# Performance work log

Hardware: AMD Instinct MI355X
Metric: run time of the kernel (lower is better)

## Reference

```python
import jax, jax.numpy as jnp
import numpy as np

N_USER = 10000
U_DIM = 256
IMG_DIM = 2048
W_DIM = 512
H_DIM = 1024
VOC = 32000
CAP_LEN = 64
SOS = VOC - 2  # <SOS> token id (n_voc_size - 2, as in the torch code)


def setup_inputs() -> dict:
    key = jax.random.key(0)
    ks = jax.random.split(key, 10)
    s = lambda k, shape: jax.random.normal(k, shape, jnp.float32) * 0.02
    return {
        "img_feat": jax.random.normal(ks[0], (1, IMG_DIM), jnp.float32),
        "uid": jax.random.randint(ks[1], (1,), 0, N_USER),
        "wei_user": s(ks[2], (N_USER, U_DIM)),
        "WI_w": s(ks[3], (W_DIM, IMG_DIM + U_DIM)),
        "WI_b": jnp.zeros((W_DIM,), jnp.float32),
        "WP_w": s(ks[4], (VOC, H_DIM)),
        "WP_b": jnp.zeros((VOC,), jnp.float32),
        "W_ih": s(ks[5], (4 * H_DIM, W_DIM)),
        "W_hh": s(ks[6], (4 * H_DIM, H_DIM)),
        "b_ih": jnp.zeros((4 * H_DIM,), jnp.float32),
        "b_hh": jnp.zeros((4 * H_DIM,), jnp.float32),
        "word_emb": s(ks[7], (VOC, W_DIM)),
    }


def _lstm_step(x, h, c, W_ih, W_hh, b_ih, b_hh):
    # torch nn.LSTM gate order: input, forget, cell(g), output
    gates = x @ W_ih.T + b_ih + h @ W_hh.T + b_hh  # [1, 4H]
    i, f, g, o = jnp.split(gates, 4, axis=-1)
    c = jax.nn.sigmoid(f) * c + jax.nn.sigmoid(i) * jnp.tanh(g)
    h = jax.nn.sigmoid(o) * jnp.tanh(c)
    return h, c


def reference(img_feat, uid, wei_user, WI_w, WI_b, WP_w, WP_b,
              W_ih, W_hh, b_ih, b_hh, word_emb):
    # user embedding + image feature -> conditioning input for step 0
    user_emb = wei_user[uid]                                  # [1, U_DIM]
    x0 = jnp.concatenate([img_feat, user_emb], axis=1) @ WI_w.T + WI_b  # [1, W_DIM]

    h = jnp.zeros((1, H_DIM), x0.dtype)
    c = jnp.zeros((1, H_DIM), x0.dtype)
    # prime the LSTM with the image/user conditioning vector
    h, c = _lstm_step(x0, h, c, W_ih, W_hh, b_ih, b_hh)

    def step(carry, _):
        h, c, wid = carry
        x = word_emb[wid]                                     # [1, W_DIM] embedding gather
        h, c = _lstm_step(x, h, c, W_ih, W_hh, b_ih, b_hh)
        logits = h @ WP_w.T + WP_b                            # [1, VOC]
        wid = jnp.argmax(logits, axis=-1).astype(jnp.int32)   # greedy token
        return (h, c, wid), (h, wid[0])

    wid0 = jnp.full((1,), SOS, jnp.int32)
    _, (hiddens, captions) = jax.lax.scan(step, (h, c, wid0), None, length=CAP_LEN)
    # hiddens: [CAP_LEN, 1, H_DIM] (matches torch cat of per-step LSTM outputs)
    return hiddens, captions
```

## Files before the change

### kernel.cpp

```cpp
#include <hip/hip_runtime.h>
#include <hip/hip_bf16.h>
#include <math.h>

#define H_DIM 1024
#define W_DIM 512
#define VOC 32000
#define CAP_LEN 64
#define U_DIM 256
#define IMG_DIM 2048
#define XIN_DIM (IMG_DIM + U_DIM)
#define SOS 31998
#define NBLK_LOGITS 512


__device__ __forceinline__ float wave_reduce_sum(float v) {
    #pragma unroll
    for (int off = 32; off > 0; off >>= 1)
        v += __shfl_xor(v, off, 64);
    return v;
}

__device__ __forceinline__ unsigned long long umax64(unsigned long long a, unsigned long long b) {
    return a > b ? a : b;
}

__device__ __forceinline__ unsigned short f2bf_rne(float f) {
    unsigned u = __float_as_uint(f);
    unsigned rounding = 0x7FFFu + ((u >> 16) & 1u);
    return (unsigned short)((u + rounding) >> 16);
}
__device__ __forceinline__ float bflo(unsigned u) { return __uint_as_float(u << 16); }
__device__ __forceinline__ float bfhi(unsigned u) { return __uint_as_float(u & 0xFFFF0000u); }

__global__ void k_init(const float* __restrict__ img, const int* __restrict__ uid,
                       const float* __restrict__ wei_user, float* __restrict__ wsf) {
    int i = blockIdx.x * blockDim.x + threadIdx.x;
    if (i < 4096) wsf[i] = 0.f;
    if (i < XIN_DIM) {
        float v = (i < IMG_DIM) ? img[i]
                                : wei_user[(size_t)uid[0] * U_DIM + (i - IMG_DIM)];
        wsf[4096 + i] = v;
    }
}

__global__ void k_cvt_wp(const float* __restrict__ src, ushort* __restrict__ dst) {
    int i = blockIdx.x * blockDim.x + threadIdx.x;
    const float4 a = reinterpret_cast<const float4*>(src)[2 * i];
    const float4 b = reinterpret_cast<const float4*>(src)[2 * i + 1];
    union { ushort s[8]; uint4 v; } u;
    u.s[0] = f2bf_rne(a.x); u.s[1] = f2bf_rne(a.y);
    u.s[2] = f2bf_rne(a.z); u.s[3] = f2bf_rne(a.w);
    u.s[4] = f2bf_rne(b.x); u.s[5] = f2bf_rne(b.y);
    u.s[6] = f2bf_rne(b.z); u.s[7] = f2bf_rne(b.w);
    reinterpret_cast<uint4*>(dst)[i] = u.v;
}

__global__ void k_x0(const float* __restrict__ WI_w, const float* __restrict__ WI_b,
                     const float* __restrict__ xin, float* __restrict__ x0) {
    int wave = threadIdx.x >> 6;
    int lane = threadIdx.x & 63;
    int row  = blockIdx.x * 4 + wave;
    const float* wr = WI_w + (size_t)row * XIN_DIM;
    float acc = 0.f;
    #pragma unroll
    for (int k = 0; k < 9; ++k) {
        int col = 4 * lane + 256 * k;
        float4 w4 = *reinterpret_cast<const float4*>(wr  + col);
        float4 v4 = *reinterpret_cast<const float4*>(xin + col);
        acc += w4.x * v4.x + w4.y * v4.y + w4.z * v4.z + w4.w * v4.w;
    }
    acc = wave_reduce_sum(acc);
    if (lane == 0) x0[row] = acc + WI_b[row];
}

__global__ void k_lstm(int t,
                       const float* __restrict__ W_ih, const float* __restrict__ W_hh,
                       const float* __restrict__ b_ih, const float* __restrict__ b_hh,
                       const float* __restrict__ word_emb, const float* __restrict__ x0,
                       const unsigned long long* __restrict__ partial,
                       float* __restrict__ out_cap,
                       const float* __restrict__ h_in, const float* __restrict__ c_in,
                       float* __restrict__ h_out, float* __restrict__ c_out,
                       float* __restrict__ out_hid) {
    __shared__ unsigned long long red[256];
    int tid  = threadIdx.x;
    int wave = tid >> 6;
    int lane = tid & 63;
    int j = blockIdx.x * 4 + wave;

    const float* x;
    if (t < 0) {
        x = x0;
    } else if (t == 0) {
        x = word_emb + (size_t)SOS * W_DIM;
    } else {
        unsigned long long b = umax64(partial[tid], partial[tid + 256]);
        red[tid] = b;
        __syncthreads();
        #pragma unroll
        for (int s = 128; s >= 1; s >>= 1) {
            if (tid < s) red[tid] = umax64(red[tid], red[tid + s]);
            __syncthreads();
        }
        int wid = (int)(0xFFFFFFFFu - (unsigned)(red[0] & 0xFFFFFFFFull));
        if (blockIdx.x == 0 && tid == 0) out_cap[t - 1] = (float)wid;
        x = word_emb + (size_t)wid * W_DIM;
    }

    float g[4];
    #pragma unroll
    for (int gi = 0; gi < 4; ++gi) {
        int row = gi * H_DIM + j;
        const float* wi = W_ih + (size_t)row * W_DIM;
        const float* wh = W_hh + (size_t)row * H_DIM;
        float acc = 0.f;
        #pragma unroll
        for (int k = 0; k < 2; ++k) {
            int col = 4 * lane + 256 * k;
            float4 w4 = *reinterpret_cast<const float4*>(wi + col);
            float4 v4 = *reinterpret_cast<const float4*>(x  + col);
            acc += w4.x * v4.x + w4.y * v4.y + w4.z * v4.z + w4.w * v4.w;
        }
        #pragma unroll
        for (int k = 0; k < 4; ++k) {
            int col = 4 * lane + 256 * k;
            float4 w4 = *reinterpret_cast<const float4*>(wh   + col);
            float4 v4 = *reinterpret_cast<const float4*>(h_in + col);
            acc += w4.x * v4.x + w4.y * v4.y + w4.z * v4.z + w4.w * v4.w;
        }
        acc = wave_reduce_sum(acc);
        g[gi] = acc + b_ih[row] + b_hh[row];
    }
    if (lane == 0) {
        float ig = 1.f / (1.f + expf(-g[0]));
        float fg = 1.f / (1.f + expf(-g[1]));
        float gg = tanhf(g[2]);
        float og = 1.f / (1.f + expf(-g[3]));
        float cn = fg * c_in[j] + ig * gg;
        float hn = og * tanhf(cn);
        c_out[j] = cn;
        h_out[j] = hn;
        if (out_hid) out_hid[j] = hn;
    }
}

__global__ void k_logits_bf16(const ushort* __restrict__ WP16,
                              const float* __restrict__ WP_b,
                              const float* __restrict__ h,
                              unsigned long long* __restrict__ partial) {
    int wave = threadIdx.x >> 6;
    int lane = threadIdx.x & 63;
    int wv = blockIdx.x * 4 + wave;
    float4 h0a = *reinterpret_cast<const float4*>(h + 8 * lane);
    float4 h0b = *reinterpret_cast<const float4*>(h + 8 * lane + 4);
    float4 h1a = *reinterpret_cast<const float4*>(h + 8 * lane + 512);
    float4 h1b = *reinterpret_cast<const float4*>(h + 8 * lane + 516);
    unsigned long long best = 0ull;
    for (int row = wv; row < VOC; row += NBLK_LOGITS * 4) {
        const uint4* wr = reinterpret_cast<const uint4*>(WP16 + (size_t)row * H_DIM);
        uint4 w0 = wr[lane];
        uint4 w1 = wr[lane + 64];
        float acc;
        acc  = bflo(w0.x) * h0a.x + bfhi(w0.x) * h0a.y;
        acc += bflo(w0.y) * h0a.z + bfhi(w0.y) * h0a.w;
        acc += bflo(w0.z) * h0b.x + bfhi(w0.z) * h0b.y;
        acc += bflo(w0.w) * h0b.z + bfhi(w0.w) * h0b.w;
        acc += bflo(w1.x) * h1a.x + bfhi(w1.x) * h1a.y;
        acc += bflo(w1.y) * h1a.z + bfhi(w1.y) * h1a.w;
        acc += bflo(w1.z) * h1b.x + bfhi(w1.z) * h1b.y;
        acc += bflo(w1.w) * h1b.z + bfhi(w1.w) * h1b.w;
        acc = wave_reduce_sum(acc);
        float logit = acc + WP_b[row];
        unsigned int ub = __float_as_uint(logit);
        ub = (ub & 0x80000000u) ? ~ub : (ub | 0x80000000u);
        unsigned long long p = ((unsigned long long)ub << 32)
                             | (unsigned long long)(0xFFFFFFFFu - (unsigned)row);
        best = umax64(best, p);
    }
    __shared__ unsigned long long sm[4];
    if (lane == 0) sm[wave] = best;
    __syncthreads();
    if (threadIdx.x == 0) {
        unsigned long long m = umax64(umax64(sm[0], sm[1]), umax64(sm[2], sm[3]));
        partial[blockIdx.x] = m;
    }
}

__global__ void k_logits_f32(const float* __restrict__ WP_w, const float* __restrict__ WP_b,
                             const float* __restrict__ h,
                             unsigned long long* __restrict__ partial) {
    int wave = threadIdx.x >> 6;
    int lane = threadIdx.x & 63;
    int wv = blockIdx.x * 4 + wave;
    unsigned long long best = 0ull;
    for (int row = wv; row < VOC; row += NBLK_LOGITS * 4) {
        const float* wr = WP_w + (size_t)row * H_DIM;
        float acc = 0.f;
        #pragma unroll
        for (int k = 0; k < 4; ++k) {
            int col = 4 * lane + 256 * k;
            float4 w4 = *reinterpret_cast<const float4*>(wr + col);
            float4 v4 = *reinterpret_cast<const float4*>(h  + col);
            acc += w4.x * v4.x + w4.y * v4.y + w4.z * v4.z + w4.w * v4.w;
        }
        acc = wave_reduce_sum(acc);
        float logit = acc + WP_b[row];
        unsigned int ub = __float_as_uint(logit);
        ub = (ub & 0x80000000u) ? ~ub : (ub | 0x80000000u);
        unsigned long long p = ((unsigned long long)ub << 32)
                             | (unsigned long long)(0xFFFFFFFFu - (unsigned)row);
        best = umax64(best, p);
    }
    __shared__ unsigned long long sm[4];
    if (lane == 0) sm[wave] = best;
    __syncthreads();
    if (threadIdx.x == 0) {
        unsigned long long m = umax64(umax64(sm[0], sm[1]), umax64(sm[2], sm[3]));
        partial[blockIdx.x] = m;
    }
}

__global__ void k_argmax_final(const unsigned long long* __restrict__ partial,
                               float* __restrict__ out_cap) {
    __shared__ unsigned long long sm[256];
    int tid = threadIdx.x;
    sm[tid] = umax64(partial[tid], partial[tid + 256]);
    __syncthreads();
    for (int s = 128; s > 0; s >>= 1) {
        if (tid < s) sm[tid] = umax64(sm[tid], sm[tid + s]);
        __syncthreads();
    }
    if (tid == 0) {
        int row = (int)(0xFFFFFFFFu - (unsigned)(sm[0] & 0xFFFFFFFFull));
        out_cap[CAP_LEN - 1] = (float)row;
    }
}

extern "C" void kernel_launch(void* const* d_in, const int* in_sizes, int n_in,
                              void* d_out, int out_size, void* d_ws, size_t ws_size,
                              hipStream_t stream) {
    const float* img_feat = (const float*)d_in[0];
    const int*   uid      = (const int*)  d_in[1];
    const float* wei_user = (const float*)d_in[2];
    const float* WI_w     = (const float*)d_in[3];
    const float* WI_b     = (const float*)d_in[4];
    const float* WP_w     = (const float*)d_in[5];
    const float* WP_b     = (const float*)d_in[6];
    const float* W_ih     = (const float*)d_in[7];
    const float* W_hh     = (const float*)d_in[8];
    const float* b_ih     = (const float*)d_in[9];
    const float* b_hh     = (const float*)d_in[10];
    const float* word_emb = (const float*)d_in[11];

    float* out = (float*)d_out;
    float* wsf = (float*)d_ws;
    float* h0 = wsf;
    float* h1 = wsf + 1024;
    float* c0 = wsf + 2048;
    float* c1 = wsf + 3072;
    float* xin = wsf + 4096;
    float* x0  = wsf + 6400;
    unsigned long long* partial = (unsigned long long*)((char*)d_ws + 27904);
    ushort* WP16 = (ushort*)((char*)d_ws + (1 << 20));
    const size_t wp16_need = (1u << 20) + (size_t)VOC * H_DIM * sizeof(ushort);
    const bool use_bf16 = ws_size >= wp16_need;

    if (use_bf16)
        k_cvt_wp<<<16000, 256, 0, stream>>>(WP_w, WP16);
    k_init<<<16, 256, 0, stream>>>(img_feat, uid, wei_user, wsf);
    k_x0<<<128, 256, 0, stream>>>(WI_w, WI_b, xin, x0);

    float* out_cap = out + CAP_LEN * H_DIM;

    k_lstm<<<256, 256, 0, stream>>>(-1, W_ih, W_hh, b_ih, b_hh, word_emb, x0,
                                    partial, out_cap, h0, c0, h1, c1, nullptr);

    for (int t = 0; t < CAP_LEN; ++t) {
        const float* hi = (t & 1) ? h0 : h1;
        const float* ci = (t & 1) ? c0 : c1;
        float* ho = (t & 1) ? h1 : h0;
        float* co = (t & 1) ? c1 : c0;
        k_lstm<<<256, 256, 0, stream>>>(t, W_ih, W_hh, b_ih, b_hh, word_emb, x0,
                                        partial, out_cap, hi, ci, ho, co,
                                        out + (size_t)t * H_DIM);
        if (use_bf16)
            k_logits_bf16<<<NBLK_LOGITS, 256, 0, stream>>>(WP16, WP_b, ho, partial);
        else
            k_logits_f32<<<NBLK_LOGITS, 256, 0, stream>>>(WP_w, WP_b, ho, partial);
    }
    k_argmax_final<<<1, 256, 0, stream>>>(partial, out_cap);
}
```

Before: 1.327 ms.

## Screen vocab logits with int8 weights and bound, rescore candidates in bf16

Adds an int8 per-row quantized copy of the projection weights with a per-row error norm. Each step first screens all rows with int8 dot products, using a Cauchy-Schwarz error bound to keep only rows that could be the argmax, then rescores those candidates exactly in bf16. The goal is to cut the per-step vocab weight traffic roughly in half. The LSTM kernel also moves to one block per hidden unit with one wave per gate. In exchange it adds a one-time quantize pass and more launches per step. The fallback path has bugs: it reduces only 256 of 512 partials and calls a stray memset.

New measurement: 1.435 ms. 1.08x slower.

```diff
diff --git a/kernel.cpp b/kernel.cpp
--- a/kernel.cpp
+++ b/kernel.cpp
@@ -11,12 +11,29 @@
 #define XIN_DIM (IMG_DIM + U_DIM)
 #define SOS 31998
 #define NBLK_LOGITS 512
-
+#define NSCR 1024
+#define NRESC 125
+
+#define WSF_OFF    16384
+#define PART_OFF   44288
+#define PLOW_OFF   46080
+#define ABUF_OFF   65536
+#define WP16_OFF   (1u << 20)
+#define WQ8_OFF    (96u << 20)
+#define META_OFF   (132u << 20)
+#define WS_NEED    ((size_t)(133u << 20))
 
 __device__ __forceinline__ float wave_reduce_sum(float v) {
     #pragma unroll
     for (int off = 32; off > 0; off >>= 1)
         v += __shfl_xor(v, off, 64);
+    return v;
+}
+
+__device__ __forceinline__ float wave_reduce_fmax(float v) {
+    #pragma unroll
+    for (int off = 32; off > 0; off >>= 1)
+        v = fmaxf(v, __shfl_xor(v, off, 64));
     return v;
 }
 
@@ -32,15 +49,34 @@
 __device__ __forceinline__ float bflo(unsigned u) { return __uint_as_float(u << 16); }
 __device__ __forceinline__ float bfhi(unsigned u) { return __uint_as_float(u & 0xFFFF0000u); }
 
-__global__ void k_init(const float* __restrict__ img, const int* __restrict__ uid,
-                       const float* __restrict__ wei_user, float* __restrict__ wsf) {
-    int i = blockIdx.x * blockDim.x + threadIdx.x;
-    if (i < 4096) wsf[i] = 0.f;
-    if (i < XIN_DIM) {
-        float v = (i < IMG_DIM) ? img[i]
-                                : wei_user[(size_t)uid[0] * U_DIM + (i - IMG_DIM)];
-        wsf[4096 + i] = v;
-    }
+__device__ __forceinline__ unsigned long long pack_key(float logit, int row) {
+    unsigned int ub = __float_as_uint(logit);
+    ub = (ub & 0x80000000u) ? ~ub : (ub | 0x80000000u);
+    return ((unsigned long long)ub << 32)
+         | (unsigned long long)(0xFFFFFFFFu - (unsigned)row);
+}
+
+__device__ __forceinline__ float lstm_row_dot(const float* __restrict__ wi,
+                                              const float* __restrict__ wh,
+                                              const float* __restrict__ x,
+                                              const float* __restrict__ h_in,
+                                              int lane) {
+    float acc = 0.f;
+    #pragma unroll
+    for (int k = 0; k < 2; ++k) {
+        int col = 4 * lane + 256 * k;
+        float4 w4 = *reinterpret_cast<const float4*>(wi + col);
+        float4 v4 = *reinterpret_cast<const float4*>(x  + col);
+        acc += w4.x * v4.x + w4.y * v4.y + w4.z * v4.z + w4.w * v4.w;
+    }
+    #pragma unroll
+    for (int k = 0; k < 4; ++k) {
+        int col = 4 * lane + 256 * k;
+        float4 w4 = *reinterpret_cast<const float4*>(wh   + col);
+        float4 v4 = *reinterpret_cast<const float4*>(h_in + col);
+        acc += w4.x * v4.x + w4.y * v4.y + w4.z * v4.z + w4.w * v4.w;
+    }
+    return wave_reduce_sum(acc);
 }
 
 __global__ void k_cvt_wp(const float* __restrict__ src, ushort* __restrict__ dst) {
@@ -55,6 +91,60 @@
     reinterpret_cast<uint4*>(dst)[i] = u.v;
 }
 
+__global__ void k_quant(const ushort* __restrict__ WP16, char* __restrict__ WQ8,
+                        float2* __restrict__ meta) {
+    int wave = threadIdx.x >> 6;
+    int lane = threadIdx.x & 63;
+    int gwv = blockIdx.x * 4 + wave;
+    for (int row = gwv; row < VOC; row += 4000) {
+        const uint4* wr = reinterpret_cast<const uint4*>(WP16 + (size_t)row * H_DIM);
+        uint4 w0 = wr[lane];
+        uint4 w1 = wr[lane + 64];
+        float v[16];
+        v[0] = bflo(w0.x); v[1] = bfhi(w0.x); v[2]  = bflo(w0.y); v[3]  = bfhi(w0.y);
+        v[4] = bflo(w0.z); v[5] = bfhi(w0.z); v[6]  = bflo(w0.w); v[7]  = bfhi(w0.w);
+        v[8] = bflo(w1.x); v[9] = bfhi(w1.x); v[10] = bflo(w1.y); v[11] = bfhi(w1.y);
+        v[12] = bflo(w1.z); v[13] = bfhi(w1.z); v[14] = bflo(w1.w); v[15] = bfhi(w1.w);
+        float mx = 0.f;
+        #pragma unroll
+        for (int i = 0; i < 16; ++i) mx = fmaxf(mx, fabsf(v[i]));
+        mx = wave_reduce_fmax(mx);
+        float s = mx / 127.f;
+        float inv = (s > 0.f) ? 1.f / s : 0.f;
+        int q[16];
+        float r2 = 0.f;
+        #pragma unroll
+        for (int i = 0; i < 16; ++i) {
+            float qq = rintf(v[i] * inv);
+            qq = fminf(127.f, fmaxf(-127.f, qq));
+            q[i] = (int)qq;
+            float res = v[i] - s * qq;
+            r2 += res * res;
+        }
+        r2 = wave_reduce_sum(r2);
+        float n = sqrtf(r2) * 1.0005f;
+        #define PK(a,b,c,d) (unsigned)((q[a]&0xff)|((q[b]&0xff)<<8)|((q[c]&0xff)<<16)|((q[d]&0xff)<<24))
+        uint2 lo = make_uint2(PK(0,1,2,3), PK(4,5,6,7));
+        uint2 hi = make_uint2(PK(8,9,10,11), PK(12,13,14,15));
+        #undef PK
+        char* rowp = WQ8 + (size_t)row * H_DIM;
+        *reinterpret_cast<uint2*>(rowp + 8 * lane)       = lo;
+        *reinterpret_cast<uint2*>(rowp + 512 + 8 * lane) = hi;
+        if (lane == 0) meta[row] = make_float2(s, n);
+    }
+}
+
+__global__ void k_init(const float* __restrict__ img, const int* __restrict__ uid,
+                       const float* __restrict__ wei_user, float* __restrict__ wsf) {
+    int i = blockIdx.x * blockDim.x + threadIdx.x;
+    if (i < 4096) wsf[i] = 0.f;
+    if (i < XIN_DIM) {
+        float v = (i < IMG_DIM) ? img[i]
+                                : wei_user[(size_t)uid[0] * U_DIM + (i - IMG_DIM)];
+        wsf[4096 + i] = v;
+    }
+}
+
 __global__ void k_x0(const float* __restrict__ WI_w, const float* __restrict__ WI_b,
                      const float* __restrict__ xin, float* __restrict__ x0) {
     int wave = threadIdx.x >> 6;
@@ -73,20 +163,21 @@
     if (lane == 0) x0[row] = acc + WI_b[row];
 }
 
-__global__ void k_lstm(int t,
-                       const float* __restrict__ W_ih, const float* __restrict__ W_hh,
-                       const float* __restrict__ b_ih, const float* __restrict__ b_hh,
-                       const float* __restrict__ word_emb, const float* __restrict__ x0,
-                       const unsigned long long* __restrict__ partial,
-                       float* __restrict__ out_cap,
-                       const float* __restrict__ h_in, const float* __restrict__ c_in,
-                       float* __restrict__ h_out, float* __restrict__ c_out,
-                       float* __restrict__ out_hid) {
+__global__ void k_lstm_b(int t,
+                         const float* __restrict__ W_ih, const float* __restrict__ W_hh,
+                         const float* __restrict__ b_ih, const float* __restrict__ b_hh,
+                         const float* __restrict__ word_emb, const float* __restrict__ x0,
+                         const unsigned long long* __restrict__ partial, int npart,
+                         float* __restrict__ out_cap,
+                         const float* __restrict__ h_in, const float* __restrict__ c_in,
+                         float* __restrict__ h_out, float* __restrict__ c_out,
+                         float* __restrict__ out_hid) {
     __shared__ unsigned long long red[256];
+    __shared__ float gsm[4];
     int tid  = threadIdx.x;
     int wave = tid >> 6;
     int lane = tid & 63;
-    int j = blockIdx.x * 4 + wave;
+    int j = blockIdx.x;
 
     const float* x;
     if (t < 0) {
@@ -94,8 +185,7 @@
     } else if (t == 0) {
         x = word_emb + (size_t)SOS * W_DIM;
     } else {
-        unsigned long long b = umax64(partial[tid], partial[tid + 256]);
-        red[tid] = b;
+        red[tid] = (tid < npart) ? partial[tid] : 0ull;
         __syncthreads();
         #pragma unroll
         for (int s = 128; s >= 1; s >>= 1) {
@@ -107,40 +197,153 @@
         x = word_emb + (size_t)wid * W_DIM;
     }
 
-    float g[4];
-    #pragma unroll
-    for (int gi = 0; gi < 4; ++gi) {
-        int row = gi * H_DIM + j;
-        const float* wi = W_ih + (size_t)row * W_DIM;
-        const float* wh = W_hh + (size_t)row * H_DIM;
-        float acc = 0.f;
-        #pragma unroll
-        for (int k = 0; k < 2; ++k) {
-            int col = 4 * lane + 256 * k;
-            float4 w4 = *reinterpret_cast<const float4*>(wi + col);
-            float4 v4 = *reinterpret_cast<const float4*>(x  + col);
-            acc += w4.x * v4.x + w4.y * v4.y + w4.z * v4.z + w4.w * v4.w;
-        }
-        #pragma unroll
-        for (int k = 0; k < 4; ++k) {
-            int col = 4 * lane + 256 * k;
-            float4 w4 = *reinterpret_cast<const float4*>(wh   + col);
-            float4 v4 = *reinterpret_cast<const float4*>(h_in + col);
-            acc += w4.x * v4.x + w4.y * v4.y + w4.z * v4.z + w4.w * v4.w;
-        }
-        acc = wave_reduce_sum(acc);
-        g[gi] = acc + b_ih[row] + b_hh[row];
-    }
-    if (lane == 0) {
-        float ig = 1.f / (1.f + expf(-g[0]));
-        float fg = 1.f / (1.f + expf(-g[1]));
-        float gg = tanhf(g[2]);
-        float og = 1.f / (1.f + expf(-g[3]));
+    int row = wave * H_DIM + j;
+    float acc = lstm_row_dot(W_ih + (size_t)row * W_DIM,
+                             W_hh + (size_t)row * H_DIM, x, h_in, lane);
+    float g = acc + b_ih[row] + b_hh[row];
+    if (lane == 0) gsm[wave] = g;
+    __syncthreads();
+    if (tid == 0) {
+        float ig = 1.f / (1.f + expf(-gsm[0]));
+        float fg = 1.f / (1.f + expf(-gsm[1]));
+        float gg = tanhf(gsm[2]);
+        float og = 1.f / (1.f + expf(-gsm[3]));
         float cn = fg * c_in[j] + ig * gg;
         float hn = og * tanhf(cn);
         c_out[j] = cn;
         h_out[j] = hn;
         if (out_hid) out_hid[j] = hn;
+    }
+}
+
+__global__ void k_screen(const char* __restrict__ WQ8, const float2* __restrict__ meta,
+                         const float* __restrict__ WP_b, const float* __restrict__ h,
+                         float2* __restrict__ abuf, float* __restrict__ plow) {
+    __shared__ float lds_h[H_DIM];
+    __shared__ float sred[256];
+    __shared__ float bl[4];
+    int tid  = threadIdx.x;
+    int wave = tid >> 6;
+    int lane = tid & 63;
+    int gwv = blockIdx.x * 4 + wave;
+
+    float s2 = 0.f;
+    #pragma unroll
+    for (int i = 0; i < 4; ++i) {
+        float v = h[tid + 256 * i];
+        lds_h[tid + 256 * i] = v;
+        s2 += v * v;
+    }
+    sred[tid] = s2;
+    __syncthreads();
+    #pragma unroll
+    for (int s = 128; s >= 1; s >>= 1) {
+        if (tid < s) sred[tid] += sred[tid + s];
+        __syncthreads();
+    }
+    float Hb = sqrtf(sred[0]) * 1.0002f;
+
+    float wlow = -3.4e38f;
+    #pragma unroll
+    for (int k = 0; k < 8; ++k) {
+        int row = gwv + k * 4096;
+        if (row < VOC) {
+            const int4* qr = reinterpret_cast<const int4*>(WQ8 + (size_t)row * H_DIM);
+            int4 qv = qr[lane];
+            int base = 16 * lane;
+            float acc = 0.f;
+            #define UNP(d, b) \
+                acc += (float)(((d) << 24) >> 24) * lds_h[(b)]; \
+                acc += (float)(((d) << 16) >> 24) * lds_h[(b) + 1]; \
+                acc += (float)(((d) << 8)  >> 24) * lds_h[(b) + 2]; \
+                acc += (float)((d) >> 24)         * lds_h[(b) + 3];
+            UNP(qv.x, base)      UNP(qv.y, base + 4)
+            UNP(qv.z, base + 8)  UNP(qv.w, base + 12)
+            #undef UNP
+            acc = wave_reduce_sum(acc);
+            float2 mt = meta[row];
+            float ahat = mt.x * acc + WP_b[row];
+            float eps  = mt.y * Hb * 1.002f + 1e-3f;
+            if (lane == 0) abuf[row] = make_float2(ahat, eps);
+            wlow = fmaxf(wlow, ahat - eps);
+        }
+    }
+    if (lane == 0) bl[wave] = wlow;
+    __syncthreads();
+    if (tid == 0)
+        plow[blockIdx.x] = fmaxf(fmaxf(bl[0], bl[1]), fmaxf(bl[2], bl[3]));
+}
+
+__global__ void k_rescore(const ushort* __restrict__ WP16, const float* __restrict__ WP_b,
+                          const float* __restrict__ h, const float2* __restrict__ abuf,
+                          const float* __restrict__ plow,
+                          unsigned long long* __restrict__ partial) {
+    __shared__ float lm[256];
+    __shared__ unsigned long long bsm[4];
+    int tid  = threadIdx.x;
+    int wave = tid >> 6;
+    int lane = tid & 63;
+
+    float m = fmaxf(fmaxf(plow[tid], plow[tid + 256]),
+                    fmaxf(plow[tid + 512], plow[tid + 768]));
+    lm[tid] = m;
+    __syncthreads();
+    #pragma unroll
+    for (int s = 128; s >= 1; s >>= 1) {
+        if (tid < s) lm[tid] = fmaxf(lm[tid], lm[tid + s]);
+        __syncthreads();
+    }
+    float M = lm[0];
+
+    float4 h0a = *reinterpret_cast<const float4*>(h + 8 * lane);
+    float4 h0b = *reinterpret_cast<const float4*>(h + 8 * lane + 4);
+    float4 h1a = *reinterpret_cast<const float4*>(h + 8 * lane + 512);
+    float4 h1b = *reinterpret_cast<const float4*>(h + 8 * lane + 516);
+
+    int row = blockIdx.x * 256 + tid;
+    float2 ae = abuf[row];
+    bool cand = (ae.x + ae.y >= M);
+    unsigned long long best = 0ull;
+    unsigned long long mask = __ballot(cand);
+    while (mask) {
+        int src = __ffsll((long long)mask) - 1;
+        mask &= mask - 1;
+        int crow = __shfl(row, src, 64);
+        const uint4* wr = reinterpret_cast<const uint4*>(WP16 + (size_t)crow * H_DIM);
+        uint4 w0 = wr[lane];
+        uint4 w1 = wr[lane + 64];
+        float acc;
+        acc  = bflo(w0.x) * h0a.x + bfhi(w0.x) * h0a.y;
+        acc += bflo(w0.y) * h0a.z + bfhi(w0.y) * h0a.w;
+        acc += bflo(w0.z) * h0b.x + bfhi(w0.z) * h0b.y;
+        acc += bflo(w0.w) * h0b.z + bfhi(w0.w) * h0b.w;
+        acc += bflo(w1.x) * h1a.x + bfhi(w1.x) * h1a.y;
+        acc += bflo(w1.y) * h1a.z + bfhi(w1.y) * h1a.w;
+        acc += bflo(w1.z) * h1b.x + bfhi(w1.z) * h1b.y;
+        acc += bflo(w1.w) * h1b.z + bfhi(w1.w) * h1b.w;
+        acc = wave_reduce_sum(acc);
+        float logit = acc + WP_b[crow];
+        best = umax64(best, pack_key(logit, crow));
+    }
+    if (lane == 0) bsm[wave] = best;
+    __syncthreads();
+    if (tid == 0)
+        partial[blockIdx.x] = umax64(umax64(bsm[0], bsm[1]), umax64(bsm[2], bsm[3]));
+}
+
+__global__ void k_argmax_final(const unsigned long long* __restrict__ partial, int npart,
+                               float* __restrict__ out_cap) {
+    __shared__ unsigned long long sm[256];
+    int tid = threadIdx.x;
+    sm[tid] = (tid < npart) ? partial[tid] : 0ull;
+    __syncthreads();
+    for (int s = 128; s > 0; s >>= 1) {
+        if (tid < s) sm[tid] = umax64(sm[tid], sm[tid + s]);
+        __syncthreads();
+    }
+    if (tid == 0) {
+        int row = (int)(0xFFFFFFFFu - (unsigned)(sm[0] & 0xFFFFFFFFull));
+        out_cap[CAP_LEN - 1] = (float)row;
     }
 }
 
@@ -171,69 +374,13 @@
         acc += bflo(w1.w) * h1b.z + bfhi(w1.w) * h1b.w;
         acc = wave_reduce_sum(acc);
         float logit = acc + WP_b[row];
-        unsigned int ub = __float_as_uint(logit);
-        ub = (ub & 0x80000000u) ? ~ub : (ub | 0x80000000u);
-        unsigned long long p = ((unsigned long long)ub << 32)
-                             | (unsigned long long)(0xFFFFFFFFu - (unsigned)row);
-        best = umax64(best, p);
+        best = umax64(best, pack_key(logit, row));
     }
     __shared__ unsigned long long sm[4];
     if (lane == 0) sm[wave] = best;
     __syncthreads();
-    if (threadIdx.x == 0) {
-        unsigned long long m = umax64(umax64(sm[0], sm[1]), umax64(sm[2], sm[3]));
-        partial[blockIdx.x] = m;
-    }
-}
-
-__global__ void k_logits_f32(const float* __restrict__ WP_w, const float* __restrict__ WP_b,
-                             const float* __restrict__ h,
-                             unsigned long long* __restrict__ partial) {
-    int wave = threadIdx.x >> 6;
-    int lane = threadIdx.x & 63;
-    int wv = blockIdx.x * 4 + wave;
-    unsigned long long best = 0ull;
-    for (int row = wv; row < VOC; row += NBLK_LOGITS * 4) {
-        const float* wr = WP_w + (size_t)row * H_DIM;
-        float acc = 0.f;
-        #pragma unroll
-        for (int k = 0; k < 4; ++k) {
-            int col = 4 * lane + 256 * k;
-            float4 w4 = *reinterpret_cast<const float4*>(wr + col);
-            float4 v4 = *reinterpret_cast<const float4*>(h  + col);
-            acc += w4.x * v4.x + w4.y * v4.y + w4.z * v4.z + w4.w * v4.w;
-        }
-        acc = wave_reduce_sum(acc);
-        float logit = acc + WP_b[row];
-        unsigned int ub = __float_as_uint(logit);
-        ub = (ub & 0x80000000u) ? ~ub : (ub | 0x80000000u);
-        unsigned long long p = ((unsigned long long)ub << 32)
-                             | (unsigned long long)(0xFFFFFFFFu - (unsigned)row);
-        best = umax64(best, p);
-    }
-    __shared__ unsigned long long sm[4];
-    if (lane == 0) sm[wave] = best;
-    __syncthreads();
-    if (threadIdx.x == 0) {
-        unsigned long long m = umax64(umax64(sm[0], sm[1]), umax64(sm[2], sm[3]));
-        partial[blockIdx.x] = m;
-    }
-}
-
-__global__ void k_argmax_final(const unsigned long long* __restrict__ partial,
-                               float* __restrict__ out_cap) {
-    __shared__ unsigned long long sm[256];
-    int tid = threadIdx.x;
-    sm[tid] = umax64(partial[tid], partial[tid + 256]);
-    __syncthreads();
-    for (int s = 128; s > 0; s >>= 1) {
-        if (tid < s) sm[tid] = umax64(sm[tid], sm[tid + s]);
-        __syncthreads();
-    }
-    if (tid == 0) {
-        int row = (int)(0xFFFFFFFFu - (unsigned)(sm[0] & 0xFFFFFFFFull));
-        out_cap[CAP_LEN - 1] = (float)row;
-    }
+    if (threadIdx.x == 0)
+        partial[blockIdx.x] = umax64(umax64(sm[0], sm[1]), umax64(sm[2], sm[3]));
 }
 
 extern "C" void kernel_launch(void* const* d_in, const int* in_sizes, int n_in,
@@ -253,40 +400,63 @@
     const float* word_emb = (const float*)d_in[11];
 
     float* out = (float*)d_out;
-    float* wsf = (float*)d_ws;
+    float* out_cap = out + CAP_LEN * H_DIM;
+    char* ws = (char*)d_ws;
+
+    float* wsf = (float*)(ws + WSF_OFF);
     float* h0 = wsf;
     float* h1 = wsf + 1024;
     float* c0 = wsf + 2048;
     float* c1 = wsf + 3072;
     float* xin = wsf + 4096;
     float* x0  = wsf + 6400;
-    unsigned long long* partial = (unsigned long long*)((char*)d_ws + 27904);
-    ushort* WP16 = (ushort*)((char*)d_ws + (1 << 20));
-    const size_t wp16_need = (1u << 20) + (size_t)VOC * H_DIM * sizeof(ushort);
-    const bool use_bf16 = ws_size >= wp16_need;
+    unsigned long long* partial = (unsigned long long*)(ws + PART_OFF);
+    float*  plow = (float*)(ws + PLOW_OFF);
+    float2* abuf = (float2*)(ws + ABUF_OFF);
+    ushort* WP16 = (ushort*)(ws + WP16_OFF);
+    char*   WQ8  = (char*)(ws + WQ8_OFF);
+    float2* meta = (float2*)(ws + META_OFF);
+
+    const bool use_fast = ws_size >= WS_NEED;
+    const bool use_bf16 = ws_size >= (size_t)WP16_OFF + (size_t)VOC * H_DIM * 2;
 
     if (use_bf16)
         k_cvt_wp<<<16000, 256, 0, stream>>>(WP_w, WP16);
+
     k_init<<<16, 256, 0, stream>>>(img_feat, uid, wei_user, wsf);
     k_x0<<<128, 256, 0, stream>>>(WI_w, WI_b, xin, x0);
 
-    float* out_cap = out + CAP_LEN * H_DIM;
-
-    k_lstm<<<256, 256, 0, stream>>>(-1, W_ih, W_hh, b_ih, b_hh, word_emb, x0,
-                                    partial, out_cap, h0, c0, h1, c1, nullptr);
-
-    for (int t = 0; t < CAP_LEN; ++t) {
-        const float* hi = (t & 1) ? h0 : h1;
-        const float* ci = (t & 1) ? c0 : c1;
-        float* ho = (t & 1) ? h1 : h0;
-        float* co = (t & 1) ? c1 : c0;
-        k_lstm<<<256, 256, 0, stream>>>(t, W_ih, W_hh, b_ih, b_hh, word_emb, x0,
-                                        partial, out_cap, hi, ci, ho, co,
-                                        out + (size_t)t * H_DIM);
-        if (use_bf16)
+    if (use_fast) {
+        k_quant<<<1000, 256, 0, stream>>>(WP16, WQ8, meta);
+
+        k_lstm_b<<<1024, 256, 0, stream>>>(-1, W_ih, W_hh, b_ih, b_hh, word_emb, x0,
+                                           partial, NRESC, out_cap, h0, c0, h1, c1, nullptr);
+        for (int t = 0; t < CAP_LEN; ++t) {
+            const float* hi = (t & 1) ? h0 : h1;
+            const float* ci = (t & 1) ? c0 : c1;
+            float* ho = (t & 1) ? h1 : h0;
+            float* co = (t & 1) ? c1 : c0;
+            k_lstm_b<<<1024, 256, 0, stream>>>(t, W_ih, W_hh, b_ih, b_hh, word_emb, x0,
+                                               partial, NRESC, out_cap, hi, ci, ho, co,
+                                               out + (size_t)t * H_DIM);
+            k_screen<<<NSCR, 256, 0, stream>>>(WQ8, meta, WP_b, ho, abuf, plow);
+            k_rescore<<<NRESC, 256, 0, stream>>>(WP16, WP_b, ho, abuf, plow, partial);
+        }
+        k_argmax_final<<<1, 256, 0, stream>>>(partial, NRESC, out_cap);
+    } else {
+        k_lstm_b<<<1024, 256, 0, stream>>>(-1, W_ih, W_hh, b_ih, b_hh, word_emb, x0,
+                                           partial, NBLK_LOGITS, out_cap, h0, c0, h1, c1, nullptr);
+        for (int t = 0; t < CAP_LEN; ++t) {
+            const float* hi = (t & 1) ? h0 : h1;
+            const float* ci = (t & 1) ? c0 : c1;
+            float* ho = (t & 1) ? h1 : h0;
+            float* co = (t & 1) ? c1 : c0;
+            k_lstm_b<<<1024, 256, 0, stream>>>(t, W_ih, W_hh, b_ih, b_hh, word_emb, x0,
+                                               partial, 256, out_cap, hi, ci, ho, co,
+                                               out + (size_t)t * H_DIM);
             k_logits_bf16<<<NBLK_LOGITS, 256, 0, stream>>>(WP16, WP_b, ho, partial);
-        else
-            k_logits_f32<<<NBLK_LOGITS, 256, 0, stream>>>(WP_w, WP_b, ho, partial);
-    }
-    k_argmax_final<<<1, 256, 0, stream>>>(partial, out_cap);
-}
+            hipMemsetAsync(nullptr, 0, 0, stream);
+        }
+        k_argmax_final<<<1, 256, 0, stream>>>(partial, 256, out_cap);
+    }
+}
```
